# Optimization experiments

Measured on AMD Instinct MI355X. Metric: run time of the kernel, lower is better.

## Reference

```python
import jax, jax.numpy as jnp
import numpy as np

NUM_HEADS = 16
HIDDEN = 1024
HEAD_DIM = HIDDEN // NUM_HEADS


def setup_inputs() -> dict:
    key = jax.random.key(0)
    ks = jax.random.split(key, 9)
    B, S, D = 2, 2048, HIDDEN
    scale = 1.0 / np.sqrt(D)
    inp = {
        "X": jax.random.normal(ks[0], (B, S, D), dtype=jnp.float32),
        "Wq": jax.random.normal(ks[1], (D, D), dtype=jnp.float32) * scale,
        "bq": jnp.zeros((D,), dtype=jnp.float32),
        "Wk": jax.random.normal(ks[2], (D, D), dtype=jnp.float32) * scale,
        "bk": jnp.zeros((D,), dtype=jnp.float32),
        "Wv": jax.random.normal(ks[3], (D, D), dtype=jnp.float32) * scale,
        "bv": jnp.zeros((D,), dtype=jnp.float32),
        "Wo": jax.random.normal(ks[4], (D, D), dtype=jnp.float32) * scale,
        "bo": jnp.zeros((D,), dtype=jnp.float32),
    }
    return inp


def _split_heads(x):
    b, s, d = x.shape
    return x.reshape(b, s, NUM_HEADS, HEAD_DIM).transpose(0, 2, 1, 3)  # [b,h,s,hd]


def reference(X, Wq, bq, Wk, bk, Wv, bv, Wo, bo):
    b, s, d = X.shape
    q = _split_heads(X @ Wq + bq)
    k = _split_heads(X @ Wk + bk)
    v = _split_heads(X @ Wv + bv)
    scores = jnp.einsum("bhqd,bhkd->bhqk", q, k) / jnp.sqrt(jnp.float32(HEAD_DIM))
    causal = jnp.tril(jnp.ones((s, s), dtype=bool))
    scores = jnp.where(causal[None, None], scores, jnp.float32(-jnp.inf))
    attn = jax.nn.softmax(scores, axis=-1)
    out = jnp.einsum("bhqk,bhkd->bhqd", attn, v)
    out = out.transpose(0, 2, 1, 3).reshape(b, s, d)
    return out @ Wo + bo
```

## Files before the change

### kernel.cpp

```cpp
#include <hip/hip_runtime.h>
#include <hip/hip_bf16.h>

#define S_LEN 2048
#define D_MODEL 1024
#define NHEAD 16
#define HDIM 64
#define BATCH 2
#define M_TOT (BATCH * S_LEN)
#define KVB 64

typedef __attribute__((ext_vector_type(4))) float f32x4;
typedef __attribute__((ext_vector_type(4))) short s16x4;
typedef __attribute__((ext_vector_type(8))) short s16x8;

#define AS1 __attribute__((address_space(1)))
#define AS3 __attribute__((address_space(3)))

#define SC2 0.18033688011112042f

__device__ inline short f2bf(float f) {
  unsigned u = __float_as_uint(f);
  return (short)((u + 0x7fffu + ((u >> 16) & 1u)) >> 16);
}

__device__ __forceinline__ unsigned cvtpk(float lo, float hi) {
  unsigned r;
  asm("v_cvt_pk_bf16_f32 %0, %1, %2" : "=v"(r) : "v"(lo), "v"(hi));
  return r;
}
__device__ __forceinline__ s16x4 pk4(float a, float b, float c, float d) {
  union { unsigned u[2]; s16x4 s; } x;
  x.u[0] = cvtpk(a, b);
  x.u[1] = cvtpk(c, d);
  return x.s;
}

__device__ __forceinline__ void gl_lds16(const short* g, short* l) {
  __builtin_amdgcn_global_load_lds((const AS1 void*)g, (AS3 void*)l, 16, 0, 0);
}

__global__ __launch_bounds__(256) void xcast_k(const float* __restrict__ X,
                                               short* __restrict__ Xb) {
  const size_t i = ((size_t)blockIdx.x * 256 + threadIdx.x) * 8;
  float4 a = *(const float4*)&X[i];
  float4 b = *(const float4*)&X[i + 4];
  s16x8 p;
  p[0] = f2bf(a.x); p[1] = f2bf(a.y); p[2] = f2bf(a.z); p[3] = f2bf(a.w);
  p[4] = f2bf(b.x); p[5] = f2bf(b.y); p[6] = f2bf(b.z); p[7] = f2bf(b.w);
  *(s16x8*)&Xb[i] = p;
}

__global__ __launch_bounds__(256) void wtrans_k(const float* __restrict__ W0,
                                                const float* __restrict__ W1,
                                                const float* __restrict__ W2,
                                                const float* __restrict__ W3,
                                                short* __restrict__ Wcat) {
  const int z = blockIdx.z;
  const float* W = z == 0 ? W0 : z == 1 ? W1 : z == 2 ? W2 : W3;
  short* Wt = Wcat + (size_t)z * D_MODEL * D_MODEL;
  const float scl = (z == 0) ? SC2 : 1.f;
  __shared__ float tile[32][33];
  const int tx = threadIdx.x, ty = threadIdx.y;
  const int n0 = blockIdx.x * 32, k0 = blockIdx.y * 32;
#pragma unroll
  for (int j = 0; j < 4; ++j)
    tile[ty + j * 8][tx] = W[(size_t)(k0 + ty + j * 8) * D_MODEL + n0 + tx];
  __syncthreads();
#pragma unroll
  for (int j = 0; j < 4; ++j)
    Wt[(size_t)(n0 + ty + j * 8) * D_MODEL + k0 + tx] =
        f2bf(tile[tx][ty + j * 8] * scl);
}

__device__ __forceinline__ void gemm_core_bf16(const short* __restrict__ A,
                                               const short* __restrict__ Bt,
                                               short* As, short* Bs,
                                               int m0, int n0,
                                               f32x4 (&acc)[4][4]) {
  const int tid = threadIdx.x;
  const int lane = tid & 63, w = tid >> 6;
  const int wm = w >> 1, wn = w & 1;
  const int lr = lane & 15, lg = lane >> 4;
  const int lr8 = lane >> 3;
  const int sl = lane & 7;
  const int scol = ((sl ^ lr8) << 3);

  auto stage = [&](int buf, int k0) {
#pragma unroll
    for (int j = 0; j < 4; ++j) {
      const int rb = j * 4 + w;
      const int row = rb * 8 + lr8;
      gl_lds16(&A[(size_t)(m0 + row) * D_MODEL + k0 + scol],
               &As[buf * 8192 + rb * 512]);
      gl_lds16(&Bt[(size_t)(n0 + row) * D_MODEL + k0 + scol],
               &Bs[buf * 8192 + rb * 512]);
    }
  };

  stage(0, 0);
  __syncthreads();

  for (int t = 0; t < D_MODEL / 64; ++t) {
    const int cur = t & 1;
    if (t + 1 < D_MODEL / 64) stage(cur ^ 1, (t + 1) * 64);
    const short* Ac = As + cur * 8192;
    const short* Bc = Bs + cur * 8192;
#pragma unroll
    for (int ks = 0; ks < 2; ++ks) {
      s16x8 af[4], bfr[4];
#pragma unroll
      for (int i = 0; i < 4; ++i) {
        const int Ra = wm * 64 + i * 16 + lr;
        const int Rb = wn * 64 + i * 16 + lr;
        af[i]  = *(const s16x8*)&Ac[Ra * 64 + ((((ks << 2) | lg) ^ (Ra & 7)) << 3)];
        bfr[i] = *(const s16x8*)&Bc[Rb * 64 + ((((ks << 2) | lg) ^ (Rb & 7)) << 3)];
      }
      __builtin_amdgcn_s_setprio(1);
#pragma unroll
      for (int mi = 0; mi < 4; ++mi)
#pragma unroll
        for (int ni = 0; ni < 4; ++ni)
          acc[mi][ni] = __builtin_amdgcn_mfma_f32_16x16x32_bf16(
              af[mi], bfr[ni], acc[mi][ni], 0, 0, 0);
      __builtin_amdgcn_s_setprio(0);
    }
    __syncthreads();
  }
}

__global__ __launch_bounds__(256) void gemm_qkv_k(
    const short* __restrict__ Xb, const short* __restrict__ Wcat,
    const float* __restrict__ bq, const float* __restrict__ bk,
    const float* __restrict__ bv, short* __restrict__ Qb,
    short* __restrict__ Kb, short* __restrict__ Vtb) {
  __shared__ short As[2 * 128 * 64];
  __shared__ short Bs[2 * 128 * 64];
  const int orig = blockIdx.x;
  const int wg = (orig & 7) * 96 + (orig >> 3);
  const int m0 = (wg / 24) * 128;
  const int n0 = (wg % 24) * 128;

  f32x4 acc[4][4] = {};
  gemm_core_bf16(Xb, Wcat, As, Bs, m0, n0, acc);

  const int z = n0 >> 10;
  const float* bias = z == 0 ? bq : z == 1 ? bk : bv;
  short* Cp = z == 0 ? Qb : z == 1 ? Kb : Vtb;
  const float bscl = (z == 0) ? SC2 : 1.f;

  const int tid = threadIdx.x, lane = tid & 63, w = tid >> 6;
  const int wm = w >> 1, wn = w & 1;
  const int lr = lane & 15, lg = lane >> 4;
#pragma unroll
  for (int ni = 0; ni < 4; ++ni) {
    const int n = n0 + wn * 64 + ni * 16 + lr;
    const float bn = bias[n & 1023] * bscl;
    const int h = (n >> 6) & 15, d = n & 63;
#pragma unroll
    for (int mi = 0; mi < 4; ++mi) {
      const int mb = m0 + wm * 64 + mi * 16 + lg * 4;
      f32x4 v = acc[mi][ni];
      if (z < 2) {
#pragma unroll
        for (int j = 0; j < 4; ++j) {
          int m = mb + j;
          int b = m >> 11, s = m & 2047;
          Cp[((size_t)((b * NHEAD + h) * S_LEN) + s) * HDIM + d] = f2bf(v[j] + bn);
        }
      } else {
        int b = mb >> 11, s = mb & 2047;
        s16x4 p;
#pragma unroll
        for (int j = 0; j < 4; ++j) p[j] = f2bf(v[j] + bn);
        *(s16x4*)&Cp[((size_t)((b * NHEAD + h) * HDIM) + d) * S_LEN + s] = p;
      }
    }
  }
}

__global__ __launch_bounds__(256) void gemm_o_k(const short* __restrict__ A,
                                                const short* __restrict__ Bt,
                                                const float* __restrict__ bias,
                                                float* __restrict__ C) {
  __shared__ short As[2 * 128 * 64];
  __shared__ short Bs[2 * 128 * 64];
  const int orig = blockIdx.x;
  const int wg = (orig & 7) * 32 + (orig >> 3);
  const int m0 = (wg >> 3) * 128;
  const int n0 = (wg & 7) * 128;

  f32x4 acc[4][4] = {};
  gemm_core_bf16(A, Bt, As, Bs, m0, n0, acc);

  const int tid = threadIdx.x, lane = tid & 63, w = tid >> 6;
  const int wm = w >> 1, wn = w & 1;
  const int lr = lane & 15, lg = lane >> 4;
#pragma unroll
  for (int ni = 0; ni < 4; ++ni) {
    const int n = n0 + wn * 64 + ni * 16 + lr;
    const float bn = bias[n];
#pragma unroll
    for (int mi = 0; mi < 4; ++mi) {
      const int mb = m0 + wm * 64 + mi * 16 + lg * 4;
      f32x4 v = acc[mi][ni];
#pragma unroll
      for (int j = 0; j < 4; ++j)
        C[(size_t)(mb + j) * D_MODEL + n] = v[j] + bn;
    }
  }
}

__global__ __launch_bounds__(256, 4) void attn_k(const short* __restrict__ Q,
                                                 const short* __restrict__ K,
                                                 const short* __restrict__ Vt,
                                                 short* __restrict__ AO) {
  __shared__ short Ks[2][KVB * HDIM];
  __shared__ short Vs[2][HDIM * KVB];
  const int tid = threadIdx.x, w = tid >> 6, lane = tid & 63;
  const int lr = lane & 15, lg = lane >> 4;
  const int orig = blockIdx.y * gridDim.x + blockIdx.x;
  const int wg = (orig & 7) * 128 + (orig >> 3);
  const int bh = wg >> 5, qi = wg & 31;
  const int qt = (bh & 1) ? qi : 31 - qi;
  const int q0 = qt * 64, nt = qt + 1;
  const int b = bh >> 4, h = bh & 15;
  const size_t headQK = (size_t)bh * S_LEN * HDIM;
  const size_t headV = (size_t)bh * HDIM * S_LEN;
  const int qrow = q0 + w * 16 + lr;

  const int l8 = lane >> 3, sl = lane & 7;
  const int scol = ((sl ^ l8) << 3);

  auto stage = [&](int kv0, int buf) {
#pragma unroll
    for (int j = 0; j < 2; ++j) {
      const int rb = w * 2 + j;
      const int row = rb * 8 + l8;
      gl_lds16(&K[headQK + (size_t)(kv0 + row) * HDIM + scol],
               &Ks[buf][rb * 512]);
      gl_lds16(&Vt[headV + (size_t)row * S_LEN + kv0 + scol],
               &Vs[buf][rb * 512]);
    }
  };

  const s16x8 qf0 = *(const s16x8*)&Q[headQK + (size_t)qrow * HDIM + lg * 8];
  const s16x8 qf1 = *(const s16x8*)&Q[headQK + (size_t)qrow * HDIM + 32 + lg * 8];

  f32x4 o[4] = {};
  float m_run = -1e30f;
  float l_part = 0.f;

  stage(0, 0);
  __syncthreads();

  for (int t = 0; t < nt; ++t) {
    if (t + 1 < nt) stage((t + 1) * KVB, (t + 1) & 1);
    const short* Kc = Ks[t & 1];
    const short* Vc = Vs[t & 1];

    f32x4 sc[4];
    __builtin_amdgcn_s_setprio(1);
#pragma unroll
    for (int g = 0; g < 4; ++g) {
      const int R = g * 16 + lr;
      const s16x8 kf0 = *(const s16x8*)&Kc[R * 64 + ((lg ^ (lr & 7)) << 3)];
      const s16x8 kf1 = *(const s16x8*)&Kc[R * 64 + (((4 | lg) ^ (lr & 7)) << 3)];
      f32x4 z = {0.f, 0.f, 0.f, 0.f};
      sc[g] = __builtin_amdgcn_mfma_f32_16x16x32_bf16(kf0, qf0, z, 0, 0, 0);
      sc[g] = __builtin_amdgcn_mfma_f32_16x16x32_bf16(kf1, qf1, sc[g], 0, 0, 0);
    }
    __builtin_amdgcn_s_setprio(0);

    if (t == nt - 1) {
      const int kv0 = t * KVB;
#pragma unroll
      for (int g = 0; g < 4; ++g)
#pragma unroll
        for (int j = 0; j < 4; ++j)
          if (kv0 + g * 16 + lg * 4 + j > qrow) sc[g][j] = -1e30f;
    }

    float mg[4];
#pragma unroll
    for (int g = 0; g < 4; ++g)
      mg[g] = fmaxf(fmaxf(sc[g][0], sc[g][1]), fmaxf(sc[g][2], sc[g][3]));
    const float tm = fmaxf(fmaxf(mg[0], mg[1]), fmaxf(mg[2], mg[3]));

    if (!__all(tm <= m_run + 8.f)) {
      float tr = fmaxf(tm, m_run);
      tr = fmaxf(tr, __shfl_xor(tr, 16));
      tr = fmaxf(tr, __shfl_xor(tr, 32));
      const float corr = exp2f(m_run - tr);
      l_part *= corr;
#pragma unroll
      for (int dc = 0; dc < 4; ++dc) o[dc] = o[dc] * corr;
      m_run = tr;
    }

    s16x4 pf[4];
#pragma unroll
    for (int g = 0; g < 4; ++g) {
      const float e0 = exp2f(sc[g][0] - m_run);
      const float e1 = exp2f(sc[g][1] - m_run);
      const float e2 = exp2f(sc[g][2] - m_run);
      const float e3 = exp2f(sc[g][3] - m_run);
      pf[g] = pk4(e0, e1, e2, e3);
      l_part += (e0 + e1) + (e2 + e3);
    }

    __builtin_amdgcn_s_setprio(1);
#pragma unroll
    for (int g = 0; g < 4; ++g)
#pragma unroll
      for (int dc = 0; dc < 4; ++dc) {
        const int row = dc * 16 + lr;
        const s16x4 vf = *(const s16x4*)&Vc[row * 64 +
            (((2 * g + (lg >> 1)) ^ (lr & 7)) << 3) + ((lg & 1) << 2)];
        o[dc] = __builtin_amdgcn_mfma_f32_16x16x16bf16_1k(vf, pf[g], o[dc], 0, 0, 0);
      }
    __builtin_amdgcn_s_setprio(0);
    __syncthreads();
  }

  float lt = l_part;
  lt += __shfl_xor(lt, 16);
  lt += __shfl_xor(lt, 32);
  const float inv = 1.f / lt;
#pragma unroll
  for (int dc = 0; dc < 4; ++dc) {
    s16x4 pk;
#pragma unroll
    for (int j = 0; j < 4; ++j) pk[j] = f2bf(o[dc][j] * inv);
    *(s16x4*)&AO[((size_t)(b * S_LEN + qrow)) * D_MODEL + h * HDIM + dc * 16 + lg * 4] = pk;
  }
}

extern "C" void kernel_launch(void* const* d_in, const int* in_sizes, int n_in,
                              void* d_out, int out_size, void* d_ws, size_t ws_size,
                              hipStream_t stream) {
  const float* X  = (const float*)d_in[0];
  const float* Wq = (const float*)d_in[1];
  const float* bq = (const float*)d_in[2];
  const float* Wk = (const float*)d_in[3];
  const float* bk = (const float*)d_in[4];
  const float* Wv = (const float*)d_in[5];
  const float* bv = (const float*)d_in[6];
  const float* Wo = (const float*)d_in[7];
  const float* bo = (const float*)d_in[8];
  (void)in_sizes; (void)n_in; (void)out_size; (void)ws_size;

  char* ws = (char*)d_ws;
  const size_t WSZ = (size_t)D_MODEL * D_MODEL * sizeof(short);
  const size_t QSZ = (size_t)M_TOT * D_MODEL * sizeof(short);
  short* Wcat = (short*)ws;
  short* Qb  = (short*)(ws + 4 * WSZ);
  short* Kb  = (short*)(ws + 4 * WSZ + QSZ);
  short* Vtb = (short*)(ws + 4 * WSZ + 2 * QSZ);
  short* AO  = (short*)(ws + 4 * WSZ + 3 * QSZ);
  short* Xb  = AO;
  short* Wto = Wcat + 3 * (size_t)D_MODEL * D_MODEL;

  xcast_k<<<dim3(M_TOT * D_MODEL / 2048), 256, 0, stream>>>(X, Xb);
  wtrans_k<<<dim3(32, 32, 4), dim3(32, 8), 0, stream>>>(Wq, Wk, Wv, Wo, Wcat);

  gemm_qkv_k<<<dim3(768), 256, 0, stream>>>(Xb, Wcat, bq, bk, bv,
                                            Qb, Kb, Vtb);

  attn_k<<<dim3(32, 32), 256, 0, stream>>>(Qb, Kb, Vtb, AO);

  gemm_o_k<<<dim3(256), 256, 0, stream>>>(AO, Wto, bo, (float*)d_out);
}
```

Measured before the change: 125.0 us.

## Retile QKV/O GEMMs and process two query tiles per attention block

The QKV GEMM moves to 128x192 tiles (512 blocks), so one tile can span the Q/K/V boundary and bias and destination are now picked per column. The O GEMM moves to 128x64 tiles (512 blocks) to raise block count and balance work across CUs. Attention now gives each block 128 query rows as two 64-row fragments that share each staged K/V tile, halving the K/V loads per query and cutting the grid to 512 blocks. The trade-off is higher register pressure, with launch bounds lowered to 3 and 2 waves, and possible load imbalance.

```diff
diff --git a/kernel.cpp b/kernel.cpp
--- a/kernel.cpp
+++ b/kernel.cpp
@@ -72,11 +72,18 @@
         f2bf(tile[tx][ty + j * 8] * scl);
 }
 
-__device__ __forceinline__ void gemm_core_bf16(const short* __restrict__ A,
-                                               const short* __restrict__ Bt,
-                                               short* As, short* Bs,
-                                               int m0, int n0,
-                                               f32x4 (&acc)[4][4]) {
+__global__ __launch_bounds__(256, 2) void gemm_qkv_k(
+    const short* __restrict__ Xb, const short* __restrict__ Wcat,
+    const float* __restrict__ bq, const float* __restrict__ bk,
+    const float* __restrict__ bv, short* __restrict__ Qb,
+    short* __restrict__ Kb, short* __restrict__ Vtb) {
+  __shared__ short As[2 * 128 * 64];
+  __shared__ short Bs[2 * 192 * 64];
+  const int orig = blockIdx.x;
+  const int wg = (orig & 7) * 64 + (orig >> 3);
+  const int m0 = (wg >> 4) * 128;
+  const int n0 = (wg & 15) * 192;
+
   const int tid = threadIdx.x;
   const int lane = tid & 63, w = tid >> 6;
   const int wm = w >> 1, wn = w & 1;
@@ -85,15 +92,22 @@
   const int sl = lane & 7;
   const int scol = ((sl ^ lr8) << 3);
 
+  f32x4 acc[4][6] = {};
+
   auto stage = [&](int buf, int k0) {
 #pragma unroll
     for (int j = 0; j < 4; ++j) {
       const int rb = j * 4 + w;
       const int row = rb * 8 + lr8;
-      gl_lds16(&A[(size_t)(m0 + row) * D_MODEL + k0 + scol],
+      gl_lds16(&Xb[(size_t)(m0 + row) * D_MODEL + k0 + scol],
                &As[buf * 8192 + rb * 512]);
-      gl_lds16(&Bt[(size_t)(n0 + row) * D_MODEL + k0 + scol],
-               &Bs[buf * 8192 + rb * 512]);
+    }
+#pragma unroll
+    for (int j = 0; j < 6; ++j) {
+      const int rb = j * 4 + w;
+      const int row = rb * 8 + lr8;
+      gl_lds16(&Wcat[(size_t)(n0 + row) * D_MODEL + k0 + scol],
+               &Bs[buf * 12288 + rb * 512]);
     }
   };
 
@@ -104,57 +118,39 @@
     const int cur = t & 1;
     if (t + 1 < D_MODEL / 64) stage(cur ^ 1, (t + 1) * 64);
     const short* Ac = As + cur * 8192;
-    const short* Bc = Bs + cur * 8192;
+    const short* Bc = Bs + cur * 12288;
 #pragma unroll
     for (int ks = 0; ks < 2; ++ks) {
-      s16x8 af[4], bfr[4];
+      s16x8 af[4], bfr[6];
 #pragma unroll
       for (int i = 0; i < 4; ++i) {
         const int Ra = wm * 64 + i * 16 + lr;
-        const int Rb = wn * 64 + i * 16 + lr;
-        af[i]  = *(const s16x8*)&Ac[Ra * 64 + ((((ks << 2) | lg) ^ (Ra & 7)) << 3)];
+        af[i] = *(const s16x8*)&Ac[Ra * 64 + ((((ks << 2) | lg) ^ (Ra & 7)) << 3)];
+      }
+#pragma unroll
+      for (int i = 0; i < 6; ++i) {
+        const int Rb = wn * 96 + i * 16 + lr;
         bfr[i] = *(const s16x8*)&Bc[Rb * 64 + ((((ks << 2) | lg) ^ (Rb & 7)) << 3)];
       }
       __builtin_amdgcn_s_setprio(1);
 #pragma unroll
       for (int mi = 0; mi < 4; ++mi)
 #pragma unroll
-        for (int ni = 0; ni < 4; ++ni)
+        for (int ni = 0; ni < 6; ++ni)
           acc[mi][ni] = __builtin_amdgcn_mfma_f32_16x16x32_bf16(
               af[mi], bfr[ni], acc[mi][ni], 0, 0, 0);
       __builtin_amdgcn_s_setprio(0);
     }
     __syncthreads();
   }
-}
-
-__global__ __launch_bounds__(256) void gemm_qkv_k(
-    const short* __restrict__ Xb, const short* __restrict__ Wcat,
-    const float* __restrict__ bq, const float* __restrict__ bk,
-    const float* __restrict__ bv, short* __restrict__ Qb,
-    short* __restrict__ Kb, short* __restrict__ Vtb) {
-  __shared__ short As[2 * 128 * 64];
-  __shared__ short Bs[2 * 128 * 64];
-  const int orig = blockIdx.x;
-  const int wg = (orig & 7) * 96 + (orig >> 3);
-  const int m0 = (wg / 24) * 128;
-  const int n0 = (wg % 24) * 128;
-
-  f32x4 acc[4][4] = {};
-  gemm_core_bf16(Xb, Wcat, As, Bs, m0, n0, acc);
-
-  const int z = n0 >> 10;
-  const float* bias = z == 0 ? bq : z == 1 ? bk : bv;
-  short* Cp = z == 0 ? Qb : z == 1 ? Kb : Vtb;
-  const float bscl = (z == 0) ? SC2 : 1.f;
-
-  const int tid = threadIdx.x, lane = tid & 63, w = tid >> 6;
-  const int wm = w >> 1, wn = w & 1;
-  const int lr = lane & 15, lg = lane >> 4;
-#pragma unroll
-  for (int ni = 0; ni < 4; ++ni) {
-    const int n = n0 + wn * 64 + ni * 16 + lr;
-    const float bn = bias[n & 1023] * bscl;
+
+#pragma unroll
+  for (int ni = 0; ni < 6; ++ni) {
+    const int n = n0 + wn * 96 + ni * 16 + lr;
+    const int z = n >> 10;
+    const float bn = (z == 0 ? bq[n & 1023] * SC2
+                             : (z == 1 ? bk[n & 1023] : bv[n & 1023]));
+    short* Cp = z == 0 ? Qb : z == 1 ? Kb : Vtb;
     const int h = (n >> 6) & 15, d = n & 63;
 #pragma unroll
     for (int mi = 0; mi < 4; ++mi) {
@@ -178,26 +174,80 @@
   }
 }
 
-__global__ __launch_bounds__(256) void gemm_o_k(const short* __restrict__ A,
-                                                const short* __restrict__ Bt,
-                                                const float* __restrict__ bias,
-                                                float* __restrict__ C) {
+__global__ __launch_bounds__(256, 2) void gemm_o_k(const short* __restrict__ A,
+                                                   const short* __restrict__ Bt,
+                                                   const float* __restrict__ bias,
+                                                   float* __restrict__ C) {
   __shared__ short As[2 * 128 * 64];
-  __shared__ short Bs[2 * 128 * 64];
+  __shared__ short Bs[2 * 64 * 64];
   const int orig = blockIdx.x;
-  const int wg = (orig & 7) * 32 + (orig >> 3);
-  const int m0 = (wg >> 3) * 128;
-  const int n0 = (wg & 7) * 128;
-
-  f32x4 acc[4][4] = {};
-  gemm_core_bf16(A, Bt, As, Bs, m0, n0, acc);
-
-  const int tid = threadIdx.x, lane = tid & 63, w = tid >> 6;
+  const int wg = (orig & 7) * 64 + (orig >> 3);
+  const int m0 = (wg >> 4) * 128;
+  const int n0 = (wg & 15) * 64;
+
+  const int tid = threadIdx.x;
+  const int lane = tid & 63, w = tid >> 6;
   const int wm = w >> 1, wn = w & 1;
   const int lr = lane & 15, lg = lane >> 4;
-#pragma unroll
-  for (int ni = 0; ni < 4; ++ni) {
-    const int n = n0 + wn * 64 + ni * 16 + lr;
+  const int lr8 = lane >> 3;
+  const int sl = lane & 7;
+  const int scol = ((sl ^ lr8) << 3);
+
+  f32x4 acc[4][2] = {};
+
+  auto stage = [&](int buf, int k0) {
+#pragma unroll
+    for (int j = 0; j < 4; ++j) {
+      const int rb = j * 4 + w;
+      const int row = rb * 8 + lr8;
+      gl_lds16(&A[(size_t)(m0 + row) * D_MODEL + k0 + scol],
+               &As[buf * 8192 + rb * 512]);
+    }
+#pragma unroll
+    for (int j = 0; j < 2; ++j) {
+      const int rb = j * 4 + w;
+      const int row = rb * 8 + lr8;
+      gl_lds16(&Bt[(size_t)(n0 + row) * D_MODEL + k0 + scol],
+               &Bs[buf * 4096 + rb * 512]);
+    }
+  };
+
+  stage(0, 0);
+  __syncthreads();
+
+  for (int t = 0; t < D_MODEL / 64; ++t) {
+    const int cur = t & 1;
+    if (t + 1 < D_MODEL / 64) stage(cur ^ 1, (t + 1) * 64);
+    const short* Ac = As + cur * 8192;
+    const short* Bc = Bs + cur * 4096;
+#pragma unroll
+    for (int ks = 0; ks < 2; ++ks) {
+      s16x8 af[4], bfr[2];
+#pragma unroll
+      for (int i = 0; i < 4; ++i) {
+        const int Ra = wm * 64 + i * 16 + lr;
+        af[i] = *(const s16x8*)&Ac[Ra * 64 + ((((ks << 2) | lg) ^ (Ra & 7)) << 3)];
+      }
+#pragma unroll
+      for (int i = 0; i < 2; ++i) {
+        const int Rb = wn * 32 + i * 16 + lr;
+        bfr[i] = *(const s16x8*)&Bc[Rb * 64 + ((((ks << 2) | lg) ^ (Rb & 7)) << 3)];
+      }
+      __builtin_amdgcn_s_setprio(1);
+#pragma unroll
+      for (int mi = 0; mi < 4; ++mi)
+#pragma unroll
+        for (int ni = 0; ni < 2; ++ni)
+          acc[mi][ni] = __builtin_amdgcn_mfma_f32_16x16x32_bf16(
+              af[mi], bfr[ni], acc[mi][ni], 0, 0, 0);
+      __builtin_amdgcn_s_setprio(0);
+    }
+    __syncthreads();
+  }
+
+#pragma unroll
+  for (int ni = 0; ni < 2; ++ni) {
+    const int n = n0 + wn * 32 + ni * 16 + lr;
     const float bn = bias[n];
 #pragma unroll
     for (int mi = 0; mi < 4; ++mi) {
@@ -210,7 +260,76 @@
   }
 }
 
-__global__ __launch_bounds__(256, 4) void attn_k(const short* __restrict__ Q,
+__device__ __forceinline__ void frag_step(const short* __restrict__ Kc,
+                                          const short* __restrict__ Vc,
+                                          int lr, int lg,
+                                          const s16x8 qf0, const s16x8 qf1,
+                                          int qrow, int kv0, bool domask,
+                                          f32x4 (&o)[4], float& m_run,
+                                          float& l_part) {
+  f32x4 sc[4];
+  __builtin_amdgcn_s_setprio(1);
+#pragma unroll
+  for (int g = 0; g < 4; ++g) {
+    const int R = g * 16 + lr;
+    const s16x8 kf0 = *(const s16x8*)&Kc[R * 64 + ((lg ^ (lr & 7)) << 3)];
+    const s16x8 kf1 = *(const s16x8*)&Kc[R * 64 + (((4 | lg) ^ (lr & 7)) << 3)];
+    f32x4 z = {0.f, 0.f, 0.f, 0.f};
+    sc[g] = __builtin_amdgcn_mfma_f32_16x16x32_bf16(kf0, qf0, z, 0, 0, 0);
+    sc[g] = __builtin_amdgcn_mfma_f32_16x16x32_bf16(kf1, qf1, sc[g], 0, 0, 0);
+  }
+  __builtin_amdgcn_s_setprio(0);
+
+  if (domask) {
+#pragma unroll
+    for (int g = 0; g < 4; ++g)
+#pragma unroll
+      for (int j = 0; j < 4; ++j)
+        if (kv0 + g * 16 + lg * 4 + j > qrow) sc[g][j] = -1e30f;
+  }
+
+  float mg[4];
+#pragma unroll
+  for (int g = 0; g < 4; ++g)
+    mg[g] = fmaxf(fmaxf(sc[g][0], sc[g][1]), fmaxf(sc[g][2], sc[g][3]));
+  const float tm = fmaxf(fmaxf(mg[0], mg[1]), fmaxf(mg[2], mg[3]));
+
+  if (!__all(tm <= m_run + 8.f)) {
+    float tr = fmaxf(tm, m_run);
+    tr = fmaxf(tr, __shfl_xor(tr, 16));
+    tr = fmaxf(tr, __shfl_xor(tr, 32));
+    const float corr = exp2f(m_run - tr);
+    l_part *= corr;
+#pragma unroll
+    for (int dc = 0; dc < 4; ++dc) o[dc] = o[dc] * corr;
+    m_run = tr;
+  }
+
+  s16x4 pf[4];
+#pragma unroll
+  for (int g = 0; g < 4; ++g) {
+    const float e0 = exp2f(sc[g][0] - m_run);
+    const float e1 = exp2f(sc[g][1] - m_run);
+    const float e2 = exp2f(sc[g][2] - m_run);
+    const float e3 = exp2f(sc[g][3] - m_run);
+    pf[g] = pk4(e0, e1, e2, e3);
+    l_part += (e0 + e1) + (e2 + e3);
+  }
+
+  __builtin_amdgcn_s_setprio(1);
+#pragma unroll
+  for (int g = 0; g < 4; ++g)
+#pragma unroll
+    for (int dc = 0; dc < 4; ++dc) {
+      const int row = dc * 16 + lr;
+      const s16x4 vf = *(const s16x4*)&Vc[row * 64 +
+          (((2 * g + (lg >> 1)) ^ (lr & 7)) << 3) + ((lg & 1) << 2)];
+      o[dc] = __builtin_amdgcn_mfma_f32_16x16x16bf16_1k(vf, pf[g], o[dc], 0, 0, 0);
+    }
+  __builtin_amdgcn_s_setprio(0);
+}
+
+__global__ __launch_bounds__(256, 3) void attn_k(const short* __restrict__ Q,
                                                  const short* __restrict__ K,
                                                  const short* __restrict__ Vt,
                                                  short* __restrict__ AO) {
@@ -218,15 +337,17 @@
   __shared__ short Vs[2][HDIM * KVB];
   const int tid = threadIdx.x, w = tid >> 6, lane = tid & 63;
   const int lr = lane & 15, lg = lane >> 4;
-  const int orig = blockIdx.y * gridDim.x + blockIdx.x;
-  const int wg = (orig & 7) * 128 + (orig >> 3);
-  const int bh = wg >> 5, qi = wg & 31;
-  const int qt = (bh & 1) ? qi : 31 - qi;
-  const int q0 = qt * 64, nt = qt + 1;
+  const int orig = blockIdx.x;
+  const int wg = (orig & 7) * 64 + (orig >> 3);
+  const int bh = wg >> 4;
+  const int u = wg & 15;
+  const int qt = (u & 1) ? (u >> 1) : 15 - (u >> 1);
+  const int q0 = qt * 128, nt = 2 * qt + 2;
   const int b = bh >> 4, h = bh & 15;
   const size_t headQK = (size_t)bh * S_LEN * HDIM;
   const size_t headV = (size_t)bh * HDIM * S_LEN;
-  const int qrow = q0 + w * 16 + lr;
+  const int rowA = q0 + w * 16 + lr;
+  const int rowB = rowA + 64;
 
   const int l8 = lane >> 3, sl = lane & 7;
   const int scol = ((sl ^ l8) << 3);
@@ -243,12 +364,13 @@
     }
   };
 
-  const s16x8 qf0 = *(const s16x8*)&Q[headQK + (size_t)qrow * HDIM + lg * 8];
-  const s16x8 qf1 = *(const s16x8*)&Q[headQK + (size_t)qrow * HDIM + 32 + lg * 8];
-
-  f32x4 o[4] = {};
-  float m_run = -1e30f;
-  float l_part = 0.f;
+  const s16x8 qfA0 = *(const s16x8*)&Q[headQK + (size_t)rowA * HDIM + lg * 8];
+  const s16x8 qfA1 = *(const s16x8*)&Q[headQK + (size_t)rowA * HDIM + 32 + lg * 8];
+  const s16x8 qfB0 = *(const s16x8*)&Q[headQK + (size_t)rowB * HDIM + lg * 8];
+  const s16x8 qfB1 = *(const s16x8*)&Q[headQK + (size_t)rowB * HDIM + 32 + lg * 8];
+
+  f32x4 oA[4] = {}, oB[4] = {};
+  float mA = -1e30f, mB = -1e30f, lA = 0.f, lB = 0.f;
 
   stage(0, 0);
   __syncthreads();
@@ -257,81 +379,29 @@
     if (t + 1 < nt) stage((t + 1) * KVB, (t + 1) & 1);
     const short* Kc = Ks[t & 1];
     const short* Vc = Vs[t & 1];
-
-    f32x4 sc[4];
-    __builtin_amdgcn_s_setprio(1);
-#pragma unroll
-    for (int g = 0; g < 4; ++g) {
-      const int R = g * 16 + lr;
-      const s16x8 kf0 = *(const s16x8*)&Kc[R * 64 + ((lg ^ (lr & 7)) << 3)];
-      const s16x8 kf1 = *(const s16x8*)&Kc[R * 64 + (((4 | lg) ^ (lr & 7)) << 3)];
-      f32x4 z = {0.f, 0.f, 0.f, 0.f};
-      sc[g] = __builtin_amdgcn_mfma_f32_16x16x32_bf16(kf0, qf0, z, 0, 0, 0);
-      sc[g] = __builtin_amdgcn_mfma_f32_16x16x32_bf16(kf1, qf1, sc[g], 0, 0, 0);
-    }
-    __builtin_amdgcn_s_setprio(0);
-
-    if (t == nt - 1) {
-      const int kv0 = t * KVB;
-#pragma unroll
-      for (int g = 0; g < 4; ++g)
-#pragma unroll
-        for (int j = 0; j < 4; ++j)
-          if (kv0 + g * 16 + lg * 4 + j > qrow) sc[g][j] = -1e30f;
-    }
-
-    float mg[4];
-#pragma unroll
-    for (int g = 0; g < 4; ++g)
-      mg[g] = fmaxf(fmaxf(sc[g][0], sc[g][1]), fmaxf(sc[g][2], sc[g][3]));
-    const float tm = fmaxf(fmaxf(mg[0], mg[1]), fmaxf(mg[2], mg[3]));
-
-    if (!__all(tm <= m_run + 8.f)) {
-      float tr = fmaxf(tm, m_run);
-      tr = fmaxf(tr, __shfl_xor(tr, 16));
-      tr = fmaxf(tr, __shfl_xor(tr, 32));
-      const float corr = exp2f(m_run - tr);
-      l_part *= corr;
-#pragma unroll
-      for (int dc = 0; dc < 4; ++dc) o[dc] = o[dc] * corr;
-      m_run = tr;
-    }
-
-    s16x4 pf[4];
-#pragma unroll
-    for (int g = 0; g < 4; ++g) {
-      const float e0 = exp2f(sc[g][0] - m_run);
-      const float e1 = exp2f(sc[g][1] - m_run);
-      const float e2 = exp2f(sc[g][2] - m_run);
-      const float e3 = exp2f(sc[g][3] - m_run);
-      pf[g] = pk4(e0, e1, e2, e3);
-      l_part += (e0 + e1) + (e2 + e3);
-    }
-
-    __builtin_amdgcn_s_setprio(1);
-#pragma unroll
-    for (int g = 0; g < 4; ++g)
-#pragma unroll
-      for (int dc = 0; dc < 4; ++dc) {
-        const int row = dc * 16 + lr;
-        const s16x4 vf = *(const s16x4*)&Vc[row * 64 +
-            (((2 * g + (lg >> 1)) ^ (lr & 7)) << 3) + ((lg & 1) << 2)];
-        o[dc] = __builtin_amdgcn_mfma_f32_16x16x16bf16_1k(vf, pf[g], o[dc], 0, 0, 0);
-      }
-    __builtin_amdgcn_s_setprio(0);
+    const int kv0 = t * KVB;
+
+    if (t < nt - 1)
+      frag_step(Kc, Vc, lr, lg, qfA0, qfA1, rowA, kv0, t == nt - 2, oA, mA, lA);
+    frag_step(Kc, Vc, lr, lg, qfB0, qfB1, rowB, kv0, t == nt - 1, oB, mB, lB);
+
     __syncthreads();
   }
 
-  float lt = l_part;
-  lt += __shfl_xor(lt, 16);
-  lt += __shfl_xor(lt, 32);
-  const float inv = 1.f / lt;
+  float ltA = lA, ltB = lB;
+  ltA += __shfl_xor(ltA, 16); ltA += __shfl_xor(ltA, 32);
+  ltB += __shfl_xor(ltB, 16); ltB += __shfl_xor(ltB, 32);
+  const float invA = 1.f / ltA, invB = 1.f / ltB;
 #pragma unroll
   for (int dc = 0; dc < 4; ++dc) {
-    s16x4 pk;
-#pragma unroll
-    for (int j = 0; j < 4; ++j) pk[j] = f2bf(o[dc][j] * inv);
-    *(s16x4*)&AO[((size_t)(b * S_LEN + qrow)) * D_MODEL + h * HDIM + dc * 16 + lg * 4] = pk;
+    s16x4 pa, pb;
+#pragma unroll
+    for (int j = 0; j < 4; ++j) {
+      pa[j] = f2bf(oA[dc][j] * invA);
+      pb[j] = f2bf(oB[dc][j] * invB);
+    }
+    *(s16x4*)&AO[((size_t)(b * S_LEN + rowA)) * D_MODEL + h * HDIM + dc * 16 + lg * 4] = pa;
+    *(s16x4*)&AO[((size_t)(b * S_LEN + rowB)) * D_MODEL + h * HDIM + dc * 16 + lg * 4] = pb;
   }
 }
 
@@ -363,10 +433,10 @@
   xcast_k<<<dim3(M_TOT * D_MODEL / 2048), 256, 0, stream>>>(X, Xb);
   wtrans_k<<<dim3(32, 32, 4), dim3(32, 8), 0, stream>>>(Wq, Wk, Wv, Wo, Wcat);
 
-  gemm_qkv_k<<<dim3(768), 256, 0, stream>>>(Xb, Wcat, bq, bk, bv,
+  gemm_qkv_k<<<dim3(512), 256, 0, stream>>>(Xb, Wcat, bq, bk, bv,
                                             Qb, Kb, Vtb);
 
-  attn_k<<<dim3(32, 32), 256, 0, stream>>>(Qb, Kb, Vtb, AO);
-
-  gemm_o_k<<<dim3(256), 256, 0, stream>>>(AO, Wto, bo, (float*)d_out);
-}
+  attn_k<<<dim3(512), 256, 0, stream>>>(Qb, Kb, Vtb, AO);
+
+  gemm_o_k<<<dim3(512), 256, 0, stream>>>(AO, Wto, bo, (float*)d_out);
+}
```

Result: slower. 141.5 us (+13.2%).
